# Kernel tuning notes

Measured on AMD Instinct MI355X. Metric: run time of the kernel, lower is better.

## Reference

```python
import jax, jax.numpy as jnp
import numpy as np

# Dims: a=1, b=8 (dispatch groups), m=256 (tokens per group), H=2048, E=8 experts,
# inter=1024 -> n = 2*inter = 2048 (fused gate+up projection width), K=2.
A, B, M, H, E, K, N = 1, 8, 256, 2048, 8, 2, 2048


def setup_inputs() -> dict:
    key = jax.random.key(0)
    k1, k2, k3 = jax.random.split(key, 3)
    hidden_4d = jax.random.normal(k1, (A, B, M, H), dtype=jnp.float32)
    sparsity = jax.random.uniform(k2, (A, B, K, E), dtype=jnp.float32)
    # learned parameter: nn.Parameter(torch.randn(1, E, H, inter*2) * 0.02)
    gate_up_proj = jax.random.normal(k3, (1, E, H, N), dtype=jnp.float32) * 0.02
    return {"hidden_4d": hidden_4d, "sparsity": sparsity, "gate_up_proj": gate_up_proj}


def reference(hidden_4d, sparsity, gate_up_proj):
    ib = gate_up_proj[0]              # [E, H, N]
    sp_mask = sparsity[:, :, 0, :]    # [A, B, E]
    # Original: out = einsum('abmk,ekn->abemn') * mask[..., None, None]; return out.sum()
    # Fused into a single contraction to a scalar (identical math, no abemn intermediate):
    # sum_{a,b,e,m,n} (sum_k h[a,b,m,k] * w[e,k,n]) * mask[a,b,e]
    per_en = jnp.einsum('abmk,ekn->aben', hidden_4d, ib)   # [A,B,E,N] (sum over m folded below)
    return jnp.einsum('aben,abe->', per_en, sp_mask)
```

## Files before the change

### kernel.cpp

```cpp
#include <hip/hip_runtime.h>

#define Bn 8
#define Mn 256
#define Hn 2048
#define En 8
#define Kn 2
#define Nn 2048

typedef float vf4 __attribute__((ext_vector_type(4)));


__global__ void reduce_kernel(const float* __restrict__ hidden,
                              const float* __restrict__ gup,
                              float* __restrict__ hs,
                              float* __restrict__ wsum) {
    const int bid = blockIdx.x;
    const int t   = threadIdx.x;
    if (bid < 128) {
        const int b   = bid >> 4;
        const int kh  = bid & 15;
        const int col = t & 31;
        const int mg  = t >> 5;
        const vf4* hp = (const vf4*)(hidden + ((size_t)b * Mn + mg * 32) * Hn)
                        + kh * 32 + col;
        vf4 a0 = 0.f, a1 = 0.f, a2 = 0.f, a3 = 0.f;
#pragma unroll
        for (int m = 0; m < 32; m += 4) {
            vf4 v0 = __builtin_nontemporal_load(hp + (size_t)(m + 0) * (Hn / 4));
            vf4 v1 = __builtin_nontemporal_load(hp + (size_t)(m + 1) * (Hn / 4));
            vf4 v2 = __builtin_nontemporal_load(hp + (size_t)(m + 2) * (Hn / 4));
            vf4 v3 = __builtin_nontemporal_load(hp + (size_t)(m + 3) * (Hn / 4));
            a0 += v0; a1 += v1; a2 += v2; a3 += v3;
        }
        vf4 s = (a0 + a1) + (a2 + a3);
        __shared__ vf4 sd[8][32];
        sd[mg][col] = s;
        __syncthreads();
        if (t < 32) {
            vf4 r = sd[0][t];
#pragma unroll
            for (int g = 1; g < 8; ++g) r += sd[g][t];
            ((vf4*)hs)[(size_t)b * (Hn / 4) + kh * 32 + t] = r;
        }
    } else {
        const int wave = (bid - 128) * 4 + (t >> 6);
        const int lane = t & 63;
        const size_t r0 = (size_t)wave * 4;
        const vf4* base = (const vf4*)gup;
        vf4 cur[8], nxt[8];
#pragma unroll
        for (int i = 0; i < 8; ++i)
            cur[i] = __builtin_nontemporal_load(base + r0 * 512 + i * 64 + lane);
        float rowsum[4];
#pragma unroll
        for (int j = 0; j < 4; ++j) {
            if (j < 3) {
#pragma unroll
                for (int i = 0; i < 8; ++i)
                    nxt[i] = __builtin_nontemporal_load(
                        base + (r0 + j + 1) * 512 + i * 64 + lane);
            }
            vf4 v = ((cur[0] + cur[1]) + (cur[2] + cur[3]))
                  + ((cur[4] + cur[5]) + (cur[6] + cur[7]));
            float s = (v.x + v.y) + (v.z + v.w);
#pragma unroll
            for (int off = 32; off > 0; off >>= 1)
                s += __shfl_down(s, off, 64);
            rowsum[j] = s;
            if (j < 3) {
#pragma unroll
                for (int i = 0; i < 8; ++i) cur[i] = nxt[i];
            }
        }
        if (lane == 0) {
            vf4 o = { rowsum[0], rowsum[1], rowsum[2], rowsum[3] };
            ((vf4*)wsum)[wave] = o;
        }
    }
}

__global__ void final_kernel(const float* __restrict__ sparsity,
                             const float* __restrict__ hs,
                             const float* __restrict__ wsum,
                             float* __restrict__ out) {
    __shared__ float sp[Bn][En];
    __shared__ float red[4];
    const int t = threadIdx.x;
    if (t < Bn * En) {
        const int b = t >> 3, e = t & 7;
        sp[b][e] = sparsity[b * (Kn * En) + e];
    }
    __syncthreads();
    float acc = 0.f;
#pragma unroll
    for (int i = 0; i < Hn / 256; ++i) {
        const int k = i * 256 + t;
        float h[Bn];
#pragma unroll
        for (int b = 0; b < Bn; ++b) h[b] = hs[b * Hn + k];
#pragma unroll
        for (int e = 0; e < En; ++e) {
            float g = 0.f;
#pragma unroll
            for (int b = 0; b < Bn; ++b) g += sp[b][e] * h[b];
            acc += wsum[e * Hn + k] * g;
        }
    }
#pragma unroll
    for (int off = 32; off > 0; off >>= 1)
        acc += __shfl_down(acc, off, 64);
    const int lane = t & 63, wave = t >> 6;
    if (lane == 0) red[wave] = acc;
    __syncthreads();
    if (t == 0) out[0] = (red[0] + red[1]) + (red[2] + red[3]);
}

extern "C" void kernel_launch(void* const* d_in, const int* in_sizes, int n_in,
                              void* d_out, int out_size, void* d_ws, size_t ws_size,
                              hipStream_t stream) {
    const float* hidden   = (const float*)d_in[0];
    const float* sparsity = (const float*)d_in[1];
    const float* gup      = (const float*)d_in[2];

    float* hs   = (float*)d_ws;
    float* wsum = hs + Bn * Hn;

    reduce_kernel<<<128 + 1024, 256, 0, stream>>>(hidden, gup, hs, wsum);
    final_kernel<<<1, 256, 0, stream>>>(sparsity, hs, wsum, (float*)d_out);
}
```

Measured before the change: 190.2 us.

## Defer weight row reductions to a separate kernel and deepen load prefetch

```diff
diff --git a/kernel.cpp b/kernel.cpp
--- a/kernel.cpp
+++ b/kernel.cpp
@@ -13,7 +13,7 @@
 __global__ void reduce_kernel(const float* __restrict__ hidden,
                               const float* __restrict__ gup,
                               float* __restrict__ hs,
-                              float* __restrict__ wsum) {
+                              float* __restrict__ partial) {
     const int bid = blockIdx.x;
     const int t   = threadIdx.x;
     if (bid < 128) {
@@ -46,36 +46,48 @@
         const int wave = (bid - 128) * 4 + (t >> 6);
         const int lane = t & 63;
         const size_t r0 = (size_t)wave * 4;
-        const vf4* base = (const vf4*)gup;
-        vf4 cur[8], nxt[8];
+        const vf4* base = (const vf4*)gup + r0 * (Nn / 4) + lane;
+        vf4 buf[2][8];
 #pragma unroll
         for (int i = 0; i < 8; ++i)
-            cur[i] = __builtin_nontemporal_load(base + r0 * 512 + i * 64 + lane);
-        float rowsum[4];
+            buf[0][i] = __builtin_nontemporal_load(base + 0 * (Nn / 4) + i * 64);
+#pragma unroll
+        for (int i = 0; i < 8; ++i)
+            buf[1][i] = __builtin_nontemporal_load(base + 1 * (Nn / 4) + i * 64);
+        float* pout = partial + r0 * 64 + lane;
 #pragma unroll
         for (int j = 0; j < 4; ++j) {
-            if (j < 3) {
-#pragma unroll
-                for (int i = 0; i < 8; ++i)
-                    nxt[i] = __builtin_nontemporal_load(
-                        base + (r0 + j + 1) * 512 + i * 64 + lane);
-            }
+            vf4* cur = buf[j & 1];
             vf4 v = ((cur[0] + cur[1]) + (cur[2] + cur[3]))
                   + ((cur[4] + cur[5]) + (cur[6] + cur[7]));
             float s = (v.x + v.y) + (v.z + v.w);
+            __builtin_nontemporal_store(s, pout + j * 64);
+            if (j < 2) {
 #pragma unroll
-            for (int off = 32; off > 0; off >>= 1)
-                s += __shfl_down(s, off, 64);
-            rowsum[j] = s;
-            if (j < 3) {
-#pragma unroll
-                for (int i = 0; i < 8; ++i) cur[i] = nxt[i];
+                for (int i = 0; i < 8; ++i)
+                    cur[i] = __builtin_nontemporal_load(
+                        base + (size_t)(j + 2) * (Nn / 4) + i * 64);
             }
         }
-        if (lane == 0) {
-            vf4 o = { rowsum[0], rowsum[1], rowsum[2], rowsum[3] };
-            ((vf4*)wsum)[wave] = o;
-        }
+    }
+}
+
+__global__ void wreduce_kernel(const float* __restrict__ partial,
+                               float* __restrict__ wsum) {
+    const int wave_g = blockIdx.x * 4 + (threadIdx.x >> 6);
+    const int lane   = threadIdx.x & 63;
+    const int r0     = wave_g * 64;
+    const vf4* p = (const vf4*)partial;
+#pragma unroll 4
+    for (int j = 0; j < 64; j += 4) {
+        vf4 v = p[(size_t)(r0 + j) * 16 + lane];
+        float s = (v.x + v.y) + (v.z + v.w);
+        s += __shfl_down(s, 8, 64);
+        s += __shfl_down(s, 4, 64);
+        s += __shfl_down(s, 2, 64);
+        s += __shfl_down(s, 1, 64);
+        if ((lane & 15) == 0)
+            wsum[r0 + j + (lane >> 4)] = s;
     }
 }
 
@@ -122,9 +134,11 @@
     const float* sparsity = (const float*)d_in[1];
     const float* gup      = (const float*)d_in[2];
 
-    float* hs   = (float*)d_ws;
-    float* wsum = hs + Bn * Hn;
+    float* hs      = (float*)d_ws;
+    float* wsum    = hs + Bn * Hn;
+    float* partial = wsum + En * Hn;
 
-    reduce_kernel<<<128 + 1024, 256, 0, stream>>>(hidden, gup, hs, wsum);
+    reduce_kernel<<<128 + 1024, 256, 0, stream>>>(hidden, gup, hs, partial);
+    wreduce_kernel<<<64, 256, 0, stream>>>(partial, wsum);
     final_kernel<<<1, 256, 0, stream>>>(sparsity, hs, wsum, (float*)d_out);
 }
```

After: 203.2 us. 1.07x slower.
